# Kernel tuning notes

Measured on AMD Instinct MI355X. Metric: run time of the kernel, lower is better.

Reference implementation:

```python
import jax, jax.numpy as jnp
import numpy as np
import math

D_MODEL, N_HEADS, D_HEAD, D_MLP = 768, 12, 64, 3072
EPS = 1e-5
IGNORE = -100000.0


def _ln(x, w, b):
    mu = jnp.mean(x, axis=-1, keepdims=True)
    xc = x - mu
    scale = jnp.sqrt(jnp.mean(xc * xc, axis=-1, keepdims=True) + EPS)
    return (xc / scale) * w + b


def _gelu_new(x):
    # GPT-2 'new' gelu
    return 0.5 * x * (1.0 + jnp.tanh(jnp.sqrt(2.0 / jnp.pi) * (x + 0.044715 * x ** 3)))


def setup_inputs() -> dict:
    key = jax.random.key(0)
    ks = jax.random.split(key, 12)
    std = 0.02
    inp = {
        "resid_pre": jax.random.normal(ks[0], (8, 1024, D_MODEL), jnp.float32),
        "W_Q": jax.random.normal(ks[1], (N_HEADS, D_MODEL, D_HEAD), jnp.float32) * std,
        "b_Q": jnp.zeros((N_HEADS, D_HEAD), jnp.float32),
        "W_K": jax.random.normal(ks[2], (N_HEADS, D_MODEL, D_HEAD), jnp.float32) * std,
        "b_K": jnp.zeros((N_HEADS, D_HEAD), jnp.float32),
        "W_V": jax.random.normal(ks[3], (N_HEADS, D_MODEL, D_HEAD), jnp.float32) * std,
        "b_V": jnp.zeros((N_HEADS, D_HEAD), jnp.float32),
        "W_O": jax.random.normal(ks[4], (N_HEADS, D_HEAD, D_MODEL), jnp.float32) * std,
        "b_O": jnp.zeros((D_MODEL,), jnp.float32),
        "ln1_w": jnp.ones((D_MODEL,), jnp.float32),
        "ln1_b": jnp.zeros((D_MODEL,), jnp.float32),
        "ln2_w": jnp.ones((D_MODEL,), jnp.float32),
        "ln2_b": jnp.zeros((D_MODEL,), jnp.float32),
        "W_in": jax.random.normal(ks[5], (D_MODEL, D_MLP), jnp.float32) * std,
        "b_in": jnp.zeros((D_MLP,), jnp.float32),
        "W_out": jax.random.normal(ks[6], (D_MLP, D_MODEL), jnp.float32) * std,
        "b_out": jnp.zeros((D_MODEL,), jnp.float32),
    }
    return inp


def reference(resid_pre, W_Q, b_Q, W_K, b_K, W_V, b_V, W_O, b_O,
              ln1_w, ln1_b, ln2_w, ln2_b, W_in, b_in, W_out, b_out):
    # ---- ln1 + attention ----
    n = _ln(resid_pre, ln1_w, ln1_b)  # [b, s, d]; broadcast over heads in einsums
    q = jnp.einsum('bsd,hde->bshe', n, W_Q) + b_Q
    k = jnp.einsum('bsd,hde->bshe', n, W_K) + b_K
    v = jnp.einsum('bsd,hde->bshe', n, W_V) + b_V
    scores = jnp.einsum('bqhe,bkhe->bhqk', q, k) / math.sqrt(D_HEAD)
    S = scores.shape[-1]
    causal = jnp.triu(jnp.ones((S, S), dtype=bool), k=1)
    scores = jnp.where(causal, IGNORE, scores)
    pattern = jax.nn.softmax(scores, axis=-1)
    z = jnp.einsum('bhqk,bkhe->bqhe', pattern, v)
    # per-head output with b_O / n_heads each (as in source), then summed over heads
    attn_per_head = jnp.einsum('bqhe,hed->bqhd', z, W_O) + b_O / N_HEADS
    attn_out = attn_per_head.sum(axis=2)  # [b, s, d]
    resid_mid = resid_pre + attn_out
    # ---- ln2 + mlp ----
    n2 = _ln(resid_mid, ln2_w, ln2_b)
    pre = jnp.einsum('bsd,dm->bsm', n2, W_in) + b_in
    post = _gelu_new(pre)
    mlp_out = jnp.einsum('bsm,md->bsd', post, W_out) + b_out
    return resid_mid + mlp_out
```

## Files before the change

kernel.cpp:

```cpp
#include <hip/hip_runtime.h>
#include <hip/hip_bf16.h>

typedef unsigned short u16;
typedef float f32x4 __attribute__((ext_vector_type(4)));
typedef __bf16 bf16x8 __attribute__((ext_vector_type(8)));
typedef unsigned short u16x8 __attribute__((ext_vector_type(8)));
typedef unsigned short u16x4 __attribute__((ext_vector_type(4)));

__device__ __forceinline__ float b2f(u16 u) {
    unsigned v = ((unsigned)u) << 16;
    return __builtin_bit_cast(float, v);
}
__device__ __forceinline__ u16 f2b(float f) {
    unsigned u = __builtin_bit_cast(unsigned, f);
    u += 0x7fffu + ((u >> 16) & 1u);
    return (u16)(u >> 16);
}
__device__ __forceinline__ bf16x8 ldfrag(const u16* p) {
    return __builtin_bit_cast(bf16x8, *(const u16x8*)p);
}
__device__ __forceinline__ f32x4 mfma16(bf16x8 a, bf16x8 b, f32x4 c) {
    return __builtin_amdgcn_mfma_f32_16x16x32_bf16(a, b, c, 0, 0, 0);
}
__device__ __forceinline__ void gload_lds16(const u16* g, u16* l) {
    __builtin_amdgcn_global_load_lds(
        (const __attribute__((address_space(1))) unsigned int*)(g),
        (__attribute__((address_space(3))) unsigned int*)(l), 16, 0, 0);
}

#define T_TOK 8192
#define DM 768
#define NH 12
#define DH 64
#define DMLP 3072
#define SEQ 1024
#define QKV_LD 2304
#define QK_LD 1536

#define OFF_WQKV ((size_t)0)
#define OFF_WO   (OFF_WQKV + (size_t)2304*768)
#define OFF_WIN  (OFF_WO   + (size_t)768*768)
#define OFF_WOUT (OFF_WIN  + (size_t)768*3072)
#define OFF_BQKV (OFF_WOUT + (size_t)3072*768)
#define P0       (OFF_BQKV + (size_t)4608)

#define SZ_N    ((size_t)T_TOK*DM)
#define SZ_QKV  ((size_t)T_TOK*QKV_LD)
#define A_NBUF   (P0)
#define A_QKV    (P0 + SZ_N)
#define A_Z      (P0 + SZ_N + SZ_QKV)
#define A_N2     (P0)
#define A_POST   (P0 + SZ_N)
#define PATHA_BYTES (((size_t)(P0 + SZ_N + SZ_QKV + SZ_N)) * 2)
#define B_Z      (P0)
#define B_QKVB   (P0 + SZ_N)
#define B_NBUF   (B_QKVB + (size_t)SEQ*QKV_LD)
#define B_N2     (P0)
#define B_POSTC  (P0 + SZ_N)

#define TT_QKV  432
#define TT_WO   (TT_QKV + 144)
#define TT_WIN  (TT_WO + 576)
#define TT_WOUT (TT_WIN + 576)

__global__ __launch_bounds__(256) void prep_kernel(
    const float* __restrict__ WQ, const float* __restrict__ WK, const float* __restrict__ WV,
    const float* __restrict__ WO, const float* __restrict__ Win, const float* __restrict__ Wout,
    const float* __restrict__ bQ, const float* __restrict__ bK, const float* __restrict__ bV,
    u16* __restrict__ Wqkv_t, u16* __restrict__ Wo_t, u16* __restrict__ Win_t,
    u16* __restrict__ Wout_t, float* __restrict__ bias_qkv)
{
    const int bid = blockIdx.x;
    const int tid = threadIdx.x;
    if (bid == TT_WOUT) {
        for (int j = tid; j < 2304; j += 256)
            bias_qkv[j] = (j < 768) ? bQ[j] : ((j < 1536) ? bK[j - 768] : bV[j - 1536]);
        return;
    }
    __shared__ u16 tile[64][72];

    const float* sp; u16* dp;
    int sldc, dldc;
    if (bid < TT_QKV) {
        int wh = bid / 12, td = bid % 12;
        int which = wh / 12, h = wh % 12;
        const float* W = (which == 0) ? WQ : ((which == 1) ? WK : WV);
        sp = W + (size_t)h * 49152 + (size_t)(td * 64) * 64;   sldc = 64;
        dp = Wqkv_t + (size_t)(which * 768 + h * 64) * 768 + td * 64; dldc = 768;
    } else if (bid < TT_WO) {
        int t2 = bid - TT_QKV, ti = t2 / 12, tj = t2 % 12;
        sp = WO + (size_t)(ti * 64) * 768 + tj * 64;           sldc = 768;
        dp = Wo_t + (size_t)(tj * 64) * 768 + ti * 64;         dldc = 768;
    } else if (bid < TT_WIN) {
        int t3 = bid - TT_WO, ti = t3 / 48, tj = t3 % 48;
        sp = Win + (size_t)(ti * 64) * 3072 + tj * 64;         sldc = 3072;
        dp = Win_t + (size_t)(tj * 64) * 768 + ti * 64;        dldc = 768;
    } else {
        int t4 = bid - TT_WIN, ti = t4 / 12, tj = t4 % 12;
        sp = Wout + (size_t)(ti * 64) * 768 + tj * 64;         sldc = 768;
        dp = Wout_t + (size_t)(tj * 64) * 3072 + ti * 64;      dldc = 3072;
    }

    {
        int r = tid >> 2, cseg = (tid & 3) * 16;
        const float* src = sp + (size_t)r * sldc + cseg;
#pragma unroll
        for (int j = 0; j < 16; j++)
            tile[cseg + j][r] = f2b(src[j]);
    }
    __syncthreads();
    {
        int r2 = tid >> 2, c2seg = (tid & 3) * 16;
        u16* dst = dp + (size_t)r2 * dldc + c2seg;
        *(u16x8*)dst       = *(const u16x8*)&tile[r2][c2seg];
        *(u16x8*)(dst + 8) = *(const u16x8*)&tile[r2][c2seg + 8];
    }
}

__global__ __launch_bounds__(256) void ln_kernel(
    const float* __restrict__ x, const float* __restrict__ w,
    const float* __restrict__ bb, u16* __restrict__ out)
{
    __shared__ float red[4];
    size_t base = (size_t)blockIdx.x * DM;
    int tid = threadIdx.x;
    float v0 = x[base + tid], v1 = x[base + tid + 256], v2 = x[base + tid + 512];
    float s = v0 + v1 + v2;
#pragma unroll
    for (int off = 32; off > 0; off >>= 1) s += __shfl_xor(s, off);
    if ((tid & 63) == 0) red[tid >> 6] = s;
    __syncthreads();
    float mu = (red[0] + red[1] + red[2] + red[3]) * (1.0f / 768.0f);
    v0 -= mu; v1 -= mu; v2 -= mu;
    float q = v0 * v0 + v1 * v1 + v2 * v2;
    __syncthreads();
#pragma unroll
    for (int off = 32; off > 0; off >>= 1) q += __shfl_xor(q, off);
    if ((tid & 63) == 0) red[tid >> 6] = q;
    __syncthreads();
    float var = (red[0] + red[1] + red[2] + red[3]) * (1.0f / 768.0f);
    float sc = rsqrtf(var + 1e-5f);
    out[base + tid]       = f2b(v0 * sc * w[tid]       + bb[tid]);
    out[base + tid + 256] = f2b(v1 * sc * w[tid + 256] + bb[tid + 256]);
    out[base + tid + 512] = f2b(v2 * sc * w[tid + 512] + bb[tid + 512]);
}

template <int EPI, int TM>
__global__ __launch_bounds__(256) void gemm_bt_kernel(
    const u16* __restrict__ A, const u16* __restrict__ BT,
    const float* __restrict__ bias, const float* __restrict__ aux,
    void* __restrict__ outp, int N, int K)
{
    __shared__ __align__(16) u16 As[3][TM * 32];
    __shared__ __align__(16) u16 Bs[3][128 * 32];
    const int tid = threadIdx.x;
    const int w = tid >> 6, l = tid & 63;
    const int lr = l & 15, lq = l >> 4;
    const int bm = blockIdx.x * TM, bn = blockIdx.y * 128;
    constexpr int MT = TM / 32;
    constexpr bool TR = (EPI != 4);
    const int wm = (w >> 1) * (TM / 2), wn = (w & 1) * 64;

    f32x4 acc[MT][4];
#pragma unroll
    for (int i = 0; i < MT; i++)
#pragma unroll
        for (int j = 0; j < 4; j++) acc[i][j] = f32x4{0.f, 0.f, 0.f, 0.f};

    const int srow_a = (TM == 128) ? (w * 32 + (l >> 2)) : (w * 16 + (l >> 2));
    const int srow_b = w * 32 + (l >> 2);
    const int scol = (l & 3) * 8;
    const u16* Ab = A  + (size_t)(bm + srow_a) * K + scol;
    const u16* Bb = BT + (size_t)(bn + srow_b) * K + scol;
    const int asd = (TM == 128) ? w * 1024 : w * 512;
    const int bsd = w * 1024;

    const int kiter = K >> 5;

#define STAGE_T(kk, s)                                                      \
    {   const int k0_ = (kk) * 32;                                          \
        gload_lds16(Ab + k0_, &As[s][asd]);                                 \
        if constexpr (TM == 128) gload_lds16(Ab + 16 * K + k0_, &As[s][asd + 512]); \
        gload_lds16(Bb + k0_,          &Bs[s][bsd]);                        \
        gload_lds16(Bb + 16 * K + k0_, &Bs[s][bsd + 512]);  }

    STAGE_T(0, 0);
    STAGE_T(1, 1);

    int cur = 0;
    for (int t = 0; t < kiter; ++t) {
        if (t + 1 < kiter) {
            if constexpr (TM == 128) asm volatile("s_waitcnt vmcnt(4)" ::: "memory");
            else                     asm volatile("s_waitcnt vmcnt(3)" ::: "memory");
        } else {
            asm volatile("s_waitcnt vmcnt(0)" ::: "memory");
        }
        __builtin_amdgcn_s_barrier();
        __builtin_amdgcn_sched_barrier(0);

        const u16* Asc = &As[cur][0];
        const u16* Bsc = &Bs[cur][0];
        bf16x8 af[MT], bf[4];
#pragma unroll
        for (int mt = 0; mt < MT; mt++) af[mt] = ldfrag(&Asc[(wm + mt * 16 + lr) * 32 + lq * 8]);
#pragma unroll
        for (int nt = 0; nt < 4; nt++) bf[nt] = ldfrag(&Bsc[(wn + nt * 16 + lr) * 32 + lq * 8]);
#pragma unroll
        for (int mt = 0; mt < MT; mt++)
#pragma unroll
            for (int nt = 0; nt < 4; nt++)
                acc[mt][nt] = TR ? mfma16(bf[nt], af[mt], acc[mt][nt])
                                 : mfma16(af[mt], bf[nt], acc[mt][nt]);

        if (t + 2 < kiter) {
            int nb = cur + 2; if (nb >= 3) nb -= 3;
            STAGE_T(t + 2, nb);
        }
        cur = (cur + 1 == 3) ? 0 : cur + 1;
    }
#undef STAGE_T

    if (EPI == 4) {
        const bool isv = (bn >= 1536);
        u16* vtg = (u16*)aux;
#pragma unroll
        for (int mt = 0; mt < MT; mt++) {
            int row0 = bm + wm + mt * 16 + lq * 4;
            if (!isv) {
#pragma unroll
                for (int r = 0; r < 4; r++) {
                    size_t ro = (size_t)(row0 + r) * QK_LD;
#pragma unroll
                    for (int nt = 0; nt < 4; nt++) {
                        int col = bn + wn + nt * 16 + lr;
                        ((u16*)outp)[ro + col] = f2b(acc[mt][nt][r] + bias[col]);
                    }
                }
            } else {
                int bloc = row0 >> 10;
                int s = row0 & 1023;
#pragma unroll
                for (int nt = 0; nt < 4; nt++) {
                    int col = bn + wn + nt * 16 + lr;
                    int he = col - 1536;
                    float bcol = bias[col];
                    u16x4 pk;
                    pk[0] = f2b(acc[mt][nt][0] + bcol);
                    pk[1] = f2b(acc[mt][nt][1] + bcol);
                    pk[2] = f2b(acc[mt][nt][2] + bcol);
                    pk[3] = f2b(acc[mt][nt][3] + bcol);
                    *(u16x4*)&vtg[(size_t)bloc * (NH * 64 * SEQ)
                                  + (size_t)he * SEQ + s] = pk;
                }
            }
        }
        return;
    }

#pragma unroll
    for (int mt = 0; mt < MT; mt++) {
        int row = bm + wm + mt * 16 + lr;
        size_t ro = (size_t)row * N;
#pragma unroll
        for (int nt = 0; nt < 4; nt++) {
            int col0 = bn + wn + nt * 16 + lq * 4;
            f32x4 v = acc[mt][nt] + *(const f32x4*)&bias[col0];
            if (EPI == 0) {
                u16x4 pk;
#pragma unroll
                for (int r = 0; r < 4; r++) pk[r] = f2b(v[r]);
                *(u16x4*)&((u16*)outp)[ro + col0] = pk;
            } else if (EPI == 2) {
                u16x4 pk;
#pragma unroll
                for (int r = 0; r < 4; r++) {
                    float x = v[r];
                    float y = 0.7978845608028654f * (x + 0.044715f * x * x * x);
                    pk[r] = f2b(x / (1.0f + __expf(-2.0f * y)));
                }
                *(u16x4*)&((u16*)outp)[ro + col0] = pk;
            } else {
                f32x4 a4 = *(const f32x4*)&aux[ro + col0];
                v += a4;
                *(f32x4*)&((float*)outp)[ro + col0] = v;
            }
        }
    }
}

__global__ __launch_bounds__(256, 5) void attn_kernel(
    const u16* __restrict__ qk, const u16* __restrict__ vtg,
    u16* __restrict__ z, int b0, int bq0)
{
    __shared__ __align__(16) u16 Ks[64 * 72];
    __shared__ __align__(16) u16 Vt[64 * 72];
    __shared__ __align__(16) u16 Ps[4][16 * 72];

    const int qt = (int)(gridDim.x - 1) - (int)blockIdx.x;
    const int bh = blockIdx.y;
    const int b = b0 + bh / NH, h = bh % NH;
    const int tid = threadIdx.x, w = tid >> 6, l = tid & 63;
    const int lr = l & 15, lq = l >> 4;
    const int qbase = qt * 64;
    const u16* qp = qk + (size_t)(b - bq0) * SEQ * QK_LD + h * 64;
    const u16* kp = qp + 768;
    const u16* vthead = vtg + ((size_t)(b - bq0) * NH + h) * (64 * SEQ);
    u16* PsW = &Ps[w][0];

    bf16x8 aq0, aq1;
    {
        const u16* qrow = qp + (size_t)(qbase + w * 16 + lr) * QK_LD + lq * 8;
        aq0 = ldfrag(qrow);
        aq1 = ldfrag(qrow + 32);
    }

    float m_i = -1e30f;
    float l_i = 0.f;
    f32x4 O[4];
#pragma unroll
    for (int i = 0; i < 4; i++) O[i] = f32x4{0.f, 0.f, 0.f, 0.f};

    const int nkt = qt + 1;
    const int srow = tid >> 2;
    const int spart = (tid & 3) * 16;

    u16x8 kreg0, kreg1, vreg0, vreg1;
    {
        const u16* ks = kp + (size_t)srow * QK_LD + spart;
        kreg0 = *(const u16x8*)ks;
        kreg1 = *(const u16x8*)(ks + 8);
        const u16* vs = vthead + (size_t)srow * SEQ + spart;
        vreg0 = *(const u16x8*)vs;
        vreg1 = *(const u16x8*)(vs + 8);
    }

    for (int kt = 0; kt < nkt; ++kt) {
        __syncthreads();
        *(u16x8*)&Ks[srow * 72 + spart]     = kreg0;
        *(u16x8*)&Ks[srow * 72 + spart + 8] = kreg1;
        *(u16x8*)&Vt[srow * 72 + spart]     = vreg0;
        *(u16x8*)&Vt[srow * 72 + spart + 8] = vreg1;
        __syncthreads();
        if (kt + 1 < nkt) {
            const u16* ks = kp + (size_t)((kt + 1) * 64 + srow) * QK_LD + spart;
            kreg0 = *(const u16x8*)ks;
            kreg1 = *(const u16x8*)(ks + 8);
            const u16* vs = vthead + (size_t)srow * SEQ + (kt + 1) * 64 + spart;
            vreg0 = *(const u16x8*)vs;
            vreg1 = *(const u16x8*)(vs + 8);
        }

        f32x4 S[4];
#pragma unroll
        for (int nt = 0; nt < 4; nt++) S[nt] = f32x4{0.f, 0.f, 0.f, 0.f};
#pragma unroll
        for (int nt = 0; nt < 4; nt++) {
            bf16x8 bk0 = ldfrag(&Ks[(nt * 16 + lr) * 72 + lq * 8]);
            bf16x8 bk1 = ldfrag(&Ks[(nt * 16 + lr) * 72 + 32 + lq * 8]);
            S[nt] = mfma16(bk0, aq0, S[nt]);
            S[nt] = mfma16(bk1, aq1, S[nt]);
        }

        const bool diag = (kt == qt);
        float mx = -1e30f;
#pragma unroll
        for (int nt = 0; nt < 4; nt++)
#pragma unroll
            for (int r = 0; r < 4; r++) {
                float sv = S[nt][r] * 0.125f;
                if (diag) sv = (nt * 16 + lq * 4 + r <= w * 16 + lr) ? sv : -1e30f;
                S[nt][r] = sv;
                mx = fmaxf(mx, sv);
            }
        mx = fmaxf(mx, __shfl_xor(mx, 16));
        mx = fmaxf(mx, __shfl_xor(mx, 32));
        float mn = fmaxf(m_i, mx);
        float alpha = __expf(m_i - mn);
        m_i = mn;
        float rs = 0.f;
#pragma unroll
        for (int nt = 0; nt < 4; nt++) {
            u16x4 pk;
#pragma unroll
            for (int r = 0; r < 4; r++) {
                float pe = __expf(S[nt][r] - mn);
                rs += pe;
                pk[r] = f2b(pe);
            }
            *(u16x4*)&PsW[lr * 72 + nt * 16 + lq * 4] = pk;
        }
        rs += __shfl_xor(rs, 16);
        rs += __shfl_xor(rs, 32);
        l_i = l_i * alpha + rs;

#pragma unroll
        for (int r = 0; r < 4; r++) {
            float ar = __shfl(alpha, (l & 48) | (lq * 4 + r));
            O[0][r] *= ar; O[1][r] *= ar; O[2][r] *= ar; O[3][r] *= ar;
        }

#pragma unroll
        for (int kq = 0; kq < 2; kq++) {
            bf16x8 ap = ldfrag(&PsW[lr * 72 + kq * 32 + lq * 8]);
#pragma unroll
            for (int ot = 0; ot < 4; ot++) {
                bf16x8 bv = ldfrag(&Vt[(ot * 16 + lr) * 72 + kq * 32 + lq * 8]);
                O[ot] = mfma16(ap, bv, O[ot]);
            }
        }
    }

    float li[4];
#pragma unroll
    for (int r = 0; r < 4; r++)
        li[r] = __shfl(l_i, (l & 48) | (lq * 4 + r));
#pragma unroll
    for (int ot = 0; ot < 4; ot++)
#pragma unroll
        for (int r = 0; r < 4; r++) {
            int q = qbase + w * 16 + lq * 4 + r;
            size_t t = (size_t)b * SEQ + q;
            z[t * DM + h * 64 + ot * 16 + lr] = f2b(O[ot][r] / li[r]);
        }
}

extern "C" void kernel_launch(void* const* d_in, const int* in_sizes, int n_in,
                              void* d_out, int out_size, void* d_ws, size_t ws_size,
                              hipStream_t stream) {
    const float* resid_pre = (const float*)d_in[0];
    const float* W_Q  = (const float*)d_in[1];
    const float* b_Q  = (const float*)d_in[2];
    const float* W_K  = (const float*)d_in[3];
    const float* b_K  = (const float*)d_in[4];
    const float* W_V  = (const float*)d_in[5];
    const float* b_V  = (const float*)d_in[6];
    const float* W_O  = (const float*)d_in[7];
    const float* b_O  = (const float*)d_in[8];
    const float* ln1w = (const float*)d_in[9];
    const float* ln1b = (const float*)d_in[10];
    const float* ln2w = (const float*)d_in[11];
    const float* ln2b = (const float*)d_in[12];
    const float* W_in  = (const float*)d_in[13];
    const float* b_in  = (const float*)d_in[14];
    const float* W_out = (const float*)d_in[15];
    const float* b_out = (const float*)d_in[16];

    u16* ws16       = (u16*)d_ws;
    u16* Wqkv_t     = ws16 + OFF_WQKV;
    u16* Wo_t       = ws16 + OFF_WO;
    u16* Win_t      = ws16 + OFF_WIN;
    u16* Wout_t     = ws16 + OFF_WOUT;
    float* bias_qkv = (float*)(ws16 + OFF_BQKV);
    float* outp  = (float*)d_out;
    float* resid = (float*)d_out;

    prep_kernel<<<TT_WOUT + 1, 256, 0, stream>>>(
        W_Q, W_K, W_V, W_O, W_in, W_out, b_Q, b_K, b_V,
        Wqkv_t, Wo_t, Win_t, Wout_t, bias_qkv);

    if (ws_size >= PATHA_BYTES) {
        u16* nbuf    = ws16 + A_NBUF;
        u16* qkbuf   = ws16 + A_QKV;
        u16* vtgA    = ws16 + A_QKV + (size_t)T_TOK * QK_LD;
        u16* zbuf    = ws16 + A_Z;
        u16* n2buf   = ws16 + A_N2;
        u16* postbuf = ws16 + A_POST;

        ln_kernel<<<T_TOK, 256, 0, stream>>>(resid_pre, ln1w, ln1b, nbuf);
        gemm_bt_kernel<4, 128><<<dim3(T_TOK / 128, QKV_LD / 128), 256, 0, stream>>>(
            nbuf, Wqkv_t, bias_qkv, (const float*)vtgA, qkbuf, QKV_LD, DM);
        attn_kernel<<<dim3(SEQ / 64, 8 * NH), 256, 0, stream>>>(qkbuf, vtgA, zbuf, 0, 0);
        gemm_bt_kernel<1, 64><<<dim3(T_TOK / 64, DM / 128), 256, 0, stream>>>(
            zbuf, Wo_t, b_O, resid_pre, resid, DM, DM);
        ln_kernel<<<T_TOK, 256, 0, stream>>>(resid, ln2w, ln2b, n2buf);
        gemm_bt_kernel<2, 128><<<dim3(T_TOK / 128, DMLP / 128), 256, 0, stream>>>(
            n2buf, Win_t, b_in, nullptr, postbuf, DMLP, DM);
        gemm_bt_kernel<3, 64><<<dim3(T_TOK / 64, DM / 128), 256, 0, stream>>>(
            postbuf, Wout_t, b_out, resid, outp, DM, DMLP);
    } else {
        u16* zbuf   = ws16 + B_Z;
        u16* qkb    = ws16 + B_QKVB;
        u16* vtgB   = qkb + (size_t)SEQ * QK_LD;
        u16* nbuf   = ws16 + B_NBUF;
        u16* n2buf  = ws16 + B_N2;
        u16* postc  = ws16 + B_POSTC;

        ln_kernel<<<T_TOK, 256, 0, stream>>>(resid_pre, ln1w, ln1b, nbuf);
        for (int b = 0; b < 8; b++) {
            gemm_bt_kernel<4, 128><<<dim3(SEQ / 128, QKV_LD / 128), 256, 0, stream>>>(
                nbuf + (size_t)b * SEQ * DM, Wqkv_t, bias_qkv, (const float*)vtgB, qkb, QKV_LD, DM);
            attn_kernel<<<dim3(SEQ / 64, NH), 256, 0, stream>>>(qkb, vtgB, zbuf, b, b);
        }
        gemm_bt_kernel<1, 64><<<dim3(T_TOK / 64, DM / 128), 256, 0, stream>>>(
            zbuf, Wo_t, b_O, resid_pre, resid, DM, DM);
        ln_kernel<<<T_TOK, 256, 0, stream>>>(resid, ln2w, ln2b, n2buf);
        for (int c = 0; c < 4; c++) {
            const size_t r0 = (size_t)c * 2048;
            gemm_bt_kernel<2, 128><<<dim3(2048 / 128, DMLP / 128), 256, 0, stream>>>(
                n2buf + r0 * DM, Win_t, b_in, nullptr, postc, DMLP, DM);
            gemm_bt_kernel<3, 64><<<dim3(2048 / 64, DM / 128), 256, 0, stream>>>(
                postc, Wout_t, b_out, resid + r0 * DM, outp + r0 * DM, DM, DMLP);
        }
    }
}
```

Baseline: 395.8 us.

## Fuse LN1 into prep kernel, fold Q scaling, remap attention grid, lazy softmax rescale

Appends LayerNorm-1 blocks to the weight-prep kernel so one launch does both jobs. Moves the 1/sqrt(d) scale into the QKV GEMM epilogue for Q columns. Remaps attention blocks so each XCD handles whole heads in order. It also adds s_setprio around the MFMA sections and skips the output rescale when no row max changes. Together these cut a launch, some per-tile ALU work and cache misses, at the cost of more branchy code and a less regular grid mapping.

```diff
diff --git a/kernel.cpp b/kernel.cpp
--- a/kernel.cpp
+++ b/kernel.cpp
@@ -68,10 +68,37 @@
     const float* __restrict__ WO, const float* __restrict__ Win, const float* __restrict__ Wout,
     const float* __restrict__ bQ, const float* __restrict__ bK, const float* __restrict__ bV,
     u16* __restrict__ Wqkv_t, u16* __restrict__ Wo_t, u16* __restrict__ Win_t,
-    u16* __restrict__ Wout_t, float* __restrict__ bias_qkv)
+    u16* __restrict__ Wout_t, float* __restrict__ bias_qkv,
+    const float* __restrict__ lnx, const float* __restrict__ lnw,
+    const float* __restrict__ lnb, u16* __restrict__ lnout)
 {
     const int bid = blockIdx.x;
     const int tid = threadIdx.x;
+
+    if (bid > TT_WOUT) {
+        __shared__ float red[4];
+        size_t base = (size_t)(bid - TT_WOUT - 1) * DM;
+        float v0 = lnx[base + tid], v1 = lnx[base + tid + 256], v2 = lnx[base + tid + 512];
+        float s = v0 + v1 + v2;
+#pragma unroll
+        for (int off = 32; off > 0; off >>= 1) s += __shfl_xor(s, off);
+        if ((tid & 63) == 0) red[tid >> 6] = s;
+        __syncthreads();
+        float mu = (red[0] + red[1] + red[2] + red[3]) * (1.0f / 768.0f);
+        v0 -= mu; v1 -= mu; v2 -= mu;
+        float q = v0 * v0 + v1 * v1 + v2 * v2;
+        __syncthreads();
+#pragma unroll
+        for (int off = 32; off > 0; off >>= 1) q += __shfl_xor(q, off);
+        if ((tid & 63) == 0) red[tid >> 6] = q;
+        __syncthreads();
+        float var = (red[0] + red[1] + red[2] + red[3]) * (1.0f / 768.0f);
+        float sc = rsqrtf(var + 1e-5f);
+        lnout[base + tid]       = f2b(v0 * sc * lnw[tid]       + lnb[tid]);
+        lnout[base + tid + 256] = f2b(v1 * sc * lnw[tid + 256] + lnb[tid + 256]);
+        lnout[base + tid + 512] = f2b(v2 * sc * lnw[tid + 512] + lnb[tid + 512]);
+        return;
+    }
     if (bid == TT_WOUT) {
         for (int j = tid; j < 2304; j += 256)
             bias_qkv[j] = (j < 768) ? bQ[j] : ((j < 1536) ? bK[j - 768] : bV[j - 1536]);
@@ -233,7 +260,9 @@
 #pragma unroll
                     for (int nt = 0; nt < 4; nt++) {
                         int col = bn + wn + nt * 16 + lr;
-                        ((u16*)outp)[ro + col] = f2b(acc[mt][nt][r] + bias[col]);
+                        float v = acc[mt][nt][r] + bias[col];
+                        if (col < 768) v *= 0.125f;
+                        ((u16*)outp)[ro + col] = f2b(v);
                     }
                 }
             } else {
@@ -296,8 +325,16 @@
     __shared__ __align__(16) u16 Vt[64 * 72];
     __shared__ __align__(16) u16 Ps[4][16 * 72];
 
-    const int qt = (int)(gridDim.x - 1) - (int)blockIdx.x;
-    const int bh = blockIdx.y;
+    int qt, bh;
+    if (gridDim.y == 96) {
+        int F = (int)(blockIdx.y * gridDim.x + blockIdx.x);
+        int xcd = F & 7, idx = F >> 3;
+        bh = xcd * 12 + (idx >> 4);
+        qt = 15 - (idx & 15);
+    } else {
+        qt = (int)(gridDim.x - 1) - (int)blockIdx.x;
+        bh = blockIdx.y;
+    }
     const int b = b0 + bh / NH, h = bh % NH;
     const int tid = threadIdx.x, w = tid >> 6, l = tid & 63;
     const int lr = l & 15, lq = l >> 4;
@@ -353,6 +390,7 @@
         f32x4 S[4];
 #pragma unroll
         for (int nt = 0; nt < 4; nt++) S[nt] = f32x4{0.f, 0.f, 0.f, 0.f};
+        __builtin_amdgcn_s_setprio(1);
 #pragma unroll
         for (int nt = 0; nt < 4; nt++) {
             bf16x8 bk0 = ldfrag(&Ks[(nt * 16 + lr) * 72 + lq * 8]);
@@ -360,6 +398,7 @@
             S[nt] = mfma16(bk0, aq0, S[nt]);
             S[nt] = mfma16(bk1, aq1, S[nt]);
         }
+        __builtin_amdgcn_s_setprio(0);
 
         const bool diag = (kt == qt);
         float mx = -1e30f;
@@ -367,16 +406,20 @@
         for (int nt = 0; nt < 4; nt++)
 #pragma unroll
             for (int r = 0; r < 4; r++) {
-                float sv = S[nt][r] * 0.125f;
+                float sv = S[nt][r];
                 if (diag) sv = (nt * 16 + lq * 4 + r <= w * 16 + lr) ? sv : -1e30f;
                 S[nt][r] = sv;
                 mx = fmaxf(mx, sv);
             }
         mx = fmaxf(mx, __shfl_xor(mx, 16));
         mx = fmaxf(mx, __shfl_xor(mx, 32));
-        float mn = fmaxf(m_i, mx);
-        float alpha = __expf(m_i - mn);
-        m_i = mn;
+        const bool need = __any(mx > m_i);
+        float mn = m_i, alpha = 1.f;
+        if (need) {
+            mn = fmaxf(m_i, mx);
+            alpha = __expf(m_i - mn);
+            m_i = mn;
+        }
         float rs = 0.f;
 #pragma unroll
         for (int nt = 0; nt < 4; nt++) {
@@ -391,14 +434,18 @@
         }
         rs += __shfl_xor(rs, 16);
         rs += __shfl_xor(rs, 32);
-        l_i = l_i * alpha + rs;
-
-#pragma unroll
-        for (int r = 0; r < 4; r++) {
-            float ar = __shfl(alpha, (l & 48) | (lq * 4 + r));
-            O[0][r] *= ar; O[1][r] *= ar; O[2][r] *= ar; O[3][r] *= ar;
-        }
-
+        if (need) {
+            l_i = l_i * alpha + rs;
+#pragma unroll
+            for (int r = 0; r < 4; r++) {
+                float ar = __shfl(alpha, (l & 48) | (lq * 4 + r));
+                O[0][r] *= ar; O[1][r] *= ar; O[2][r] *= ar; O[3][r] *= ar;
+            }
+        } else {
+            l_i += rs;
+        }
+
+        __builtin_amdgcn_s_setprio(1);
 #pragma unroll
         for (int kq = 0; kq < 2; kq++) {
             bf16x8 ap = ldfrag(&PsW[lr * 72 + kq * 32 + lq * 8]);
@@ -408,6 +455,7 @@
                 O[ot] = mfma16(ap, bv, O[ot]);
             }
         }
+        __builtin_amdgcn_s_setprio(0);
     }
 
     float li[4];
@@ -454,10 +502,6 @@
     float* outp  = (float*)d_out;
     float* resid = (float*)d_out;
 
-    prep_kernel<<<TT_WOUT + 1, 256, 0, stream>>>(
-        W_Q, W_K, W_V, W_O, W_in, W_out, b_Q, b_K, b_V,
-        Wqkv_t, Wo_t, Win_t, Wout_t, bias_qkv);
-
     if (ws_size >= PATHA_BYTES) {
         u16* nbuf    = ws16 + A_NBUF;
         u16* qkbuf   = ws16 + A_QKV;
@@ -466,7 +510,10 @@
         u16* n2buf   = ws16 + A_N2;
         u16* postbuf = ws16 + A_POST;
 
-        ln_kernel<<<T_TOK, 256, 0, stream>>>(resid_pre, ln1w, ln1b, nbuf);
+        prep_kernel<<<TT_WOUT + 1 + T_TOK, 256, 0, stream>>>(
+            W_Q, W_K, W_V, W_O, W_in, W_out, b_Q, b_K, b_V,
+            Wqkv_t, Wo_t, Win_t, Wout_t, bias_qkv,
+            resid_pre, ln1w, ln1b, nbuf);
         gemm_bt_kernel<4, 128><<<dim3(T_TOK / 128, QKV_LD / 128), 256, 0, stream>>>(
             nbuf, Wqkv_t, bias_qkv, (const float*)vtgA, qkbuf, QKV_LD, DM);
         attn_kernel<<<dim3(SEQ / 64, 8 * NH), 256, 0, stream>>>(qkbuf, vtgA, zbuf, 0, 0);
@@ -485,7 +532,10 @@
         u16* n2buf  = ws16 + B_N2;
         u16* postc  = ws16 + B_POSTC;
 
-        ln_kernel<<<T_TOK, 256, 0, stream>>>(resid_pre, ln1w, ln1b, nbuf);
+        prep_kernel<<<TT_WOUT + 1 + T_TOK, 256, 0, stream>>>(
+            W_Q, W_K, W_V, W_O, W_in, W_out, b_Q, b_K, b_V,
+            Wqkv_t, Wo_t, Win_t, Wout_t, bias_qkv,
+            resid_pre, ln1w, ln1b, nbuf);
         for (int b = 0; b < 8; b++) {
             gemm_bt_kernel<4, 128><<<dim3(SEQ / 128, QKV_LD / 128), 256, 0, stream>>>(
                 nbuf + (size_t)b * SEQ * DM, Wqkv_t, bias_qkv, (const float*)vtgB, qkb, QKV_LD, DM);
```

After: 381.6 us. 3.6% less time.
